# Optimization experiments

Measured on AMD Instinct MI355X. Metric: run time of the kernel, lower is better.

Reference implementation:

```python
import jax, jax.numpy as jnp
import numpy as np

NEG = -1e9  # large negative for masked logits (TRT uses dtype min)

def _rotate_every_two(x):
    # pairs (x0,x1) -> (-x1, x0), interleaved along last dim
    xr = x.reshape(*x.shape[:-1], -1, 2)
    rot = jnp.stack([-xr[..., 1], xr[..., 0]], axis=-1)
    return rot.reshape(x.shape)

def _apply_rope(x, cos, sin):
    # rot_dim == cos.shape[-1]; here it equals the full inner dim
    rot_dim = cos.shape[-1]
    x_rot, x_pass = x[..., :rot_dim], x[..., rot_dim:]
    x_rot = x_rot * cos + _rotate_every_two(x_rot) * sin
    return jnp.concatenate([x_rot, x_pass], axis=-1) if x_pass.shape[-1] else x_rot

def setup_inputs() -> dict:
    key = jax.random.key(0)
    ks = jax.random.split(key, 12)
    B, N, D_MODEL, H, DH = 2, 2048, 1024, 16, 64
    INNER = H * DH
    x = jax.random.normal(ks[0], (B, N, D_MODEL), dtype=jnp.float32)
    # rope angles: build realistic cos/sin tables repeated per head
    pos = jnp.arange(N, dtype=jnp.float32)
    inv = 1.0 / (10000.0 ** (jnp.arange(0, DH, 2, dtype=jnp.float32) / DH))
    ang = pos[:, None] * inv[None, :]              # [N, DH/2]
    ang = jnp.repeat(ang, 2, axis=-1)              # [N, DH] interleaved pairs
    ang = jnp.tile(ang, (1, H))                    # [N, INNER]
    rope_cos = jnp.broadcast_to(jnp.cos(ang)[None], (B, N, INNER)).astype(jnp.float32)
    rope_sin = jnp.broadcast_to(jnp.sin(ang)[None], (B, N, INNER)).astype(jnp.float32)
    input_lengths = jax.random.randint(ks[1], (B,), N // 2, N + 1, dtype=jnp.int32)
    s = 1.0 / np.sqrt(D_MODEL)
    Wq = jax.random.normal(ks[2], (D_MODEL, INNER), dtype=jnp.float32) * s
    bq = jnp.zeros((INNER,), jnp.float32)
    Wk = jax.random.normal(ks[3], (D_MODEL, INNER), dtype=jnp.float32) * s
    bk = jnp.zeros((INNER,), jnp.float32)
    Wv = jax.random.normal(ks[4], (D_MODEL, INNER), dtype=jnp.float32) * s
    bv = jnp.zeros((INNER,), jnp.float32)
    Wo = jax.random.normal(ks[5], (INNER, D_MODEL), dtype=jnp.float32) * (1.0 / np.sqrt(INNER))
    bo = jnp.zeros((D_MODEL,), jnp.float32)
    return {"x": x, "rope_cos": rope_cos, "rope_sin": rope_sin,
            "input_lengths": input_lengths,
            "Wq": Wq, "bq": bq, "Wk": Wk, "bk": bk, "Wv": Wv, "bv": bv,
            "Wo": Wo, "bo": bo}

def reference(x, rope_cos, rope_sin, input_lengths, Wq, bq, Wk, bk, Wv, bv, Wo, bo):
    B, N, _ = x.shape
    H, DH = 16, 64
    q = x @ Wq + bq
    k = x @ Wk + bk
    v = x @ Wv + bv
    q = _apply_rope(q, rope_cos, rope_sin)
    k = _apply_rope(k, rope_cos, rope_sin)
    # split heads: [B,N,H,DH] -> [B,H,N,DH]
    q = q.reshape(B, N, H, DH).transpose(0, 2, 1, 3)
    k = k.reshape(B, N, H, DH).transpose(0, 2, 1, 3)
    v = v.reshape(B, N, H, DH).transpose(0, 2, 1, 3)
    # NOTE: faithful to the non-plugin source path, q is NOT pre-scaled
    scores = jnp.einsum('bhqd,bhkd->bhqk', q, k)
    key_mask = jnp.arange(N)[None, :] < input_lengths[:, None]  # [B,N]
    scores = scores + jnp.where(key_mask, 0.0, NEG).astype(scores.dtype)[:, None, None, :]
    probs = jax.nn.softmax(scores, axis=-1)
    ctx = jnp.einsum('bhqk,bhkd->bhqd', probs, v)  # [B,H,N,DH]
    ctx = ctx.transpose(0, 2, 1, 3).reshape(B, N, H * DH)
    out = ctx @ Wo + bo
    out = out * key_mask[..., None].astype(out.dtype)
    return out
```

## Files before the change

kernel.cpp:

```cpp
#include <hip/hip_runtime.h>
#include <hip/hip_bf16.h>


typedef _Float16 f16x8 __attribute__((ext_vector_type(8)));
typedef float f32x4 __attribute__((ext_vector_type(4)));

#define NEGBIG (-1.0e9f)

__device__ inline f32x4 mfma16(f16x8 a, f16x8 b, f32x4 c) {
  return __builtin_amdgcn_mfma_f32_16x16x32_f16(a, b, c, 0, 0, 0);
}

__device__ inline void gload16(const void* g, void* l) {
  __builtin_amdgcn_global_load_lds(
      (const __attribute__((address_space(1))) void*)g,
      (__attribute__((address_space(3))) void*)l, 16, 0, 0);
}

__global__ __launch_bounds__(256) void prep_kernel(
    const float* __restrict__ x, const float* __restrict__ Wq,
    const float* __restrict__ Wk, const float* __restrict__ Wv,
    const float* __restrict__ Wo, _Float16* __restrict__ xh,
    _Float16* __restrict__ wt) {
  __shared__ float tile[32][33];
  const int z = blockIdx.z;
  const int tx = threadIdx.x, ty = threadIdx.y;
  if (z == 4) {
    const int bid = blockIdx.y * 32 + blockIdx.x;
    const int t = ty * 32 + tx;
#pragma unroll
    for (int i = 0; i < 4; ++i) {
      const int o = bid * 1024 + i * 256 + t;
      const float4 v = ((const float4*)x)[o];
      union { _Float16 h[4]; short4 s; } u;
      u.h[0] = (_Float16)v.x; u.h[1] = (_Float16)v.y;
      u.h[2] = (_Float16)v.z; u.h[3] = (_Float16)v.w;
      ((short4*)xh)[o] = u.s;
    }
    return;
  }
  const float* W = (z == 0) ? Wq : (z == 1) ? Wk : (z == 2) ? Wv : Wo;
  _Float16* dh = wt + (size_t)z * 1024 * 1024;
  const int j0 = blockIdx.x * 32, k0 = blockIdx.y * 32;
  for (int i = ty; i < 32; i += 8)
    tile[i][tx] = W[(size_t)(k0 + i) * 1024 + j0 + tx];
  __syncthreads();
  for (int i = ty; i < 32; i += 8)
    dh[(size_t)(j0 + i) * 1024 + k0 + tx] = (_Float16)tile[tx][i];
}


template <int TM, int EPI>
__global__ __launch_bounds__(256) void gemm_kernel(
    const _Float16* __restrict__ A, const _Float16* __restrict__ B,
    const float* __restrict__ bias0, const float* __restrict__ bias1,
    const float* __restrict__ bias2,
    const float* __restrict__ ropeC, const float* __restrict__ ropeS,
    const int* __restrict__ lens,
    _Float16* __restrict__ outQK, _Float16* __restrict__ outVT,
    float* __restrict__ outF) {
  constexpr int MI = TM / 32;
  __shared__ __align__(16) _Float16 smem[(TM + 128) * 32];
  const int t = threadIdx.x;
  const int w = t >> 6, lane = t & 63;
  const int wr = w >> 1, wc = w & 1;
  const int fr = lane & 15, fg = lane >> 4;
  const int mtile = blockIdx.x, ntile = blockIdx.y;

  const int srow = t >> 2;
  const int skel = (t & 3) << 3;
  const size_t aBase = (size_t)(mtile * TM + srow) * 1024 + skel;
  const size_t bBase = (size_t)(ntile * 128 + srow) * 1024 + skel;
  const int ldst = t * 8;
  _Float16* lA = &smem[0];
  _Float16* lB = &smem[TM * 32];

  f32x4 acc[MI][4];
#pragma unroll
  for (int i = 0; i < MI; ++i)
#pragma unroll
    for (int j = 0; j < 4; ++j) {
      acc[i][j][0] = 0.f; acc[i][j][1] = 0.f; acc[i][j][2] = 0.f; acc[i][j][3] = 0.f;
    }

  for (int k0 = 0; k0 < 1024; k0 += 32) {
    gload16(A + aBase + k0, lA + ldst);
    if constexpr (TM == 128) gload16(A + aBase + k0 + 64 * 1024, lA + ldst + 2048);
    gload16(B + bBase + k0, lB + ldst);
    gload16(B + bBase + k0 + 64 * 1024, lB + ldst + 2048);
    __syncthreads();

    f16x8 af[MI], bf[4];
#pragma unroll
    for (int mi = 0; mi < MI; ++mi)
      af[mi] = *(const f16x8*)&lA[(wr * (TM / 2) + mi * 16 + fr) * 32 + fg * 8];
#pragma unroll
    for (int ni = 0; ni < 4; ++ni)
      bf[ni] = *(const f16x8*)&lB[(wc * 64 + ni * 16 + fr) * 32 + fg * 8];
#pragma unroll
    for (int mi = 0; mi < MI; ++mi)
#pragma unroll
      for (int ni = 0; ni < 4; ++ni)
        acc[mi][ni] = mfma16(af[mi], bf[ni], acc[mi][ni]);
    __syncthreads();
  }

  const int rowbase = mtile * TM + wr * (TM / 2);
  const int colbase = ntile * 128 + wc * 64;

  if constexpr (EPI == 0) {
    const int which = colbase >> 10;
    if (which < 2) {
      const float* bias = which ? bias1 : bias0;
#pragma unroll
      for (int ni = 0; ni < 4; ++ni) {
        const int gcol = colbase + ni * 16 + fr;
        const int jj = gcol & 1023;
        const int hh = jj >> 6, dd = jj & 63;
        const float bv = bias[jj];
#pragma unroll
        for (int mi = 0; mi < MI; ++mi) {
#pragma unroll
          for (int r = 0; r < 4; ++r) {
            const int grow = rowbase + mi * 16 + fg * 4 + r;
            const int b = grow >> 11, n = grow & 2047;
            float val = acc[mi][ni][r] + bv;
            float part = __shfl_xor(val, 1);
            const size_t ro = (size_t)(b * 2048 + n) * 1024 + jj;
            const float c = ropeC[ro], s = ropeS[ro];
            float rot = (fr & 1) ? (val * c + part * s) : (val * c - part * s);
            if (!which) rot *= 1.44269504f;
            outQK[((size_t)((which * 2 + b) * 16 + hh) * 2048 + n) * 64 + dd] =
                (_Float16)rot;
          }
        }
      }
    } else {
#pragma unroll
      for (int ni = 0; ni < 4; ++ni) {
        const int gcol = colbase + ni * 16 + fr;
        const int jj = gcol & 1023;
        const int hh = jj >> 6, dd = jj & 63;
        const float bv = bias2[jj];
#pragma unroll
        for (int mi = 0; mi < MI; ++mi) {
          const int n0 = rowbase + mi * 16 + fg * 4;
          const int b = n0 >> 11, n = n0 & 2047;
          union { _Float16 h[4]; short4 s4; } u;
#pragma unroll
          for (int r = 0; r < 4; ++r) u.h[r] = (_Float16)(acc[mi][ni][r] + bv);
          *(short4*)(outVT + ((size_t)(b * 16 + hh) * 64 + dd) * 2048 + n) = u.s4;
        }
      }
    }
  } else {
    const int b = rowbase >> 11;
    const int len = lens[b];
#pragma unroll
    for (int ni = 0; ni < 4; ++ni) {
      const int gcol = colbase + ni * 16 + fr;
      const float bv = bias0[gcol];
#pragma unroll
      for (int mi = 0; mi < MI; ++mi) {
#pragma unroll
        for (int r = 0; r < 4; ++r) {
          const int m = rowbase + mi * 16 + fg * 4 + r;
          const int n = m & 2047;
          float val = acc[mi][ni][r] + bv;
          if (n >= len) val = 0.f;
          outF[(size_t)m * 1024 + gcol] = val;
        }
      }
    }
  }
}

__global__ __launch_bounds__(128, 4) void attn_kernel(
    const _Float16* __restrict__ qk, const _Float16* __restrict__ vt,
    const int* __restrict__ lens, _Float16* __restrict__ ctx) {
  __shared__ __align__(16) char lds[18432];
  const int t = threadIdx.x;
  const int w = t >> 6, lane = t & 63;
  const int fr = lane & 15, fg = lane >> 4;
  const int qtile = blockIdx.x, bh = blockIdx.y;
  const int b = bh >> 4, h = bh & 15;
  const int len = lens[b];
  const int q0 = qtile * 32 + w * 16;
  const size_t qoff = (size_t)(b * 16 + h) * 2048 * 64;
  const size_t koff = (size_t)((2 + b) * 16 + h) * 2048 * 64;
  const size_t voff = (size_t)(b * 16 + h) * 64 * 2048;

  f16x8 qf[2];
#pragma unroll
  for (int s = 0; s < 2; ++s)
    qf[s] = *(const f16x8*)(qk + qoff + (size_t)(q0 + fr) * 64 + s * 32 + fg * 8);

  f16x8 onef;
#pragma unroll
  for (int i = 0; i < 8; ++i) onef[i] = (_Float16)1.0f;

  const int skey = t >> 3;
  const int soct = (t & 7) ^ (skey & 7);
  const size_t kg = koff + (size_t)skey * 64 + soct * 8;
  const int sd = t >> 2;
  const int svo = (t & 3) ^ ((sd >> 1) & 3);
  const size_t vg = voff + (size_t)sd * 2048 + svo * 8;
  char* pb = lds + 16384 + w * 1024;

  f32x4 o_acc[4];
#pragma unroll
  for (int dt = 0; dt < 4; ++dt) {
    o_acc[dt][0] = 0.f; o_acc[dt][1] = 0.f; o_acc[dt][2] = 0.f; o_acc[dt][3] = 0.f;
  }
  f32x4 lacc;
  lacc[0] = 0.f; lacc[1] = 0.f; lacc[2] = 0.f; lacc[3] = 0.f;
  float mrun = -1e30f;

#define STAGE(bi, k0_) do { \
    char* dst = lds + (bi) * 8192 + t * 16; \
    gload16(qk + kg + (size_t)(k0_) * 64, dst); \
    gload16(qk + kg + (size_t)(k0_) * 64 + 1024, dst + 2048); \
    gload16(vt + vg + (k0_), dst + 4096); \
    gload16(vt + vg + (k0_) + 32 * 2048, dst + 6144); \
  } while (0)

  const int nkb = (len + 31) >> 5;
  STAGE(0, 0);

  for (int kb = 0; kb < nkb; ++kb) {
    const int cur = kb & 1;
    if (kb + 1 < nkb) {
      STAGE(cur ^ 1, (kb + 1) * 32);
      asm volatile("s_waitcnt vmcnt(4)" ::: "memory");
    } else {
      asm volatile("s_waitcnt vmcnt(0)" ::: "memory");
    }
    __builtin_amdgcn_s_barrier();

    const char* Kb = lds + cur * 8192;
    const char* Vb = Kb + 4096;

    f32x4 sacc[2];
#pragma unroll
    for (int ct = 0; ct < 2; ++ct) {
      sacc[ct][0] = 0.f; sacc[ct][1] = 0.f; sacc[ct][2] = 0.f; sacc[ct][3] = 0.f;
    }
    __builtin_amdgcn_s_setprio(1);
#pragma unroll
    for (int ct = 0; ct < 2; ++ct) {
      const int krow = ct * 16 + fr;
      const int swz = (krow & 7) << 4;
#pragma unroll
      for (int s = 0; s < 2; ++s) {
        const f16x8 kf = *(const f16x8*)(Kb + ((krow * 128 + s * 64 + fg * 16) ^ swz));
        sacc[ct] = mfma16(kf, qf[s], sacc[ct]);
      }
    }
    __builtin_amdgcn_s_setprio(0);

    if ((kb == nkb - 1) && (len & 31)) {
#pragma unroll
      for (int ct = 0; ct < 2; ++ct)
#pragma unroll
        for (int r = 0; r < 4; ++r)
          if (kb * 32 + ct * 16 + fg * 4 + r >= len) sacc[ct][r] = NEGBIG;
    }

    float mx = fmaxf(fmaxf(fmaxf(sacc[0][0], sacc[0][1]), fmaxf(sacc[0][2], sacc[0][3])),
                     fmaxf(fmaxf(sacc[1][0], sacc[1][1]), fmaxf(sacc[1][2], sacc[1][3])));
    mx = fmaxf(mx, __shfl_xor(mx, 16));
    mx = fmaxf(mx, __shfl_xor(mx, 32));
    if (!__all(mx <= mrun + 8.f)) {
      const float mnew = fmaxf(mrun, mx);
      const float scq = exp2f(mrun - mnew);
      mrun = mnew;
      float scrow[4];
#pragma unroll
      for (int r = 0; r < 4; ++r) scrow[r] = __shfl(scq, fg * 4 + r);
      lacc[0] *= scrow[0]; lacc[1] *= scrow[1];
      lacc[2] *= scrow[2]; lacc[3] *= scrow[3];
#pragma unroll
      for (int dt = 0; dt < 4; ++dt) {
        o_acc[dt][0] *= scrow[0]; o_acc[dt][1] *= scrow[1];
        o_acc[dt][2] *= scrow[2]; o_acc[dt][3] *= scrow[3];
      }
    }
    float p[2][4];
#pragma unroll
    for (int ct = 0; ct < 2; ++ct)
#pragma unroll
      for (int r = 0; r < 4; ++r) p[ct][r] = exp2f(sacc[ct][r] - mrun);

    const int pswz = ((fr >> 1) & 3) << 4;
#pragma unroll
    for (int ct = 0; ct < 2; ++ct) {
      union { _Float16 h[4]; uint2 u2; } pk;
      pk.h[0] = (_Float16)p[ct][0]; pk.h[1] = (_Float16)p[ct][1];
      pk.h[2] = (_Float16)p[ct][2]; pk.h[3] = (_Float16)p[ct][3];
      *(uint2*)(pb + ((fr * 64 + ct * 32 + fg * 8) ^ pswz)) = pk.u2;
    }
    const f16x8 pf = *(const f16x8*)(pb + ((fr * 64 + fg * 16) ^ pswz));

    __builtin_amdgcn_s_setprio(1);
#pragma unroll
    for (int dt = 0; dt < 4; ++dt) {
      const int d = dt * 16 + fr;
      const f16x8 vf =
          *(const f16x8*)(Vb + ((d * 64 + (fg ^ ((d >> 1) & 3)) * 16)));
      o_acc[dt] = mfma16(pf, vf, o_acc[dt]);
    }
    lacc = mfma16(pf, onef, lacc);
    __builtin_amdgcn_s_setprio(0);

    asm volatile("" ::: "memory");
    __builtin_amdgcn_s_barrier();
  }
#undef STAGE

  float linv[4];
#pragma unroll
  for (int r = 0; r < 4; ++r) linv[r] = 1.f / lacc[r];
#pragma unroll
  for (int dt = 0; dt < 4; ++dt)
#pragma unroll
    for (int r = 0; r < 4; ++r) {
      const int n = q0 + fg * 4 + r;
      ctx[(size_t)(b * 2048 + n) * 1024 + h * 64 + dt * 16 + fr] =
          (_Float16)(o_acc[dt][r] * linv[r]);
    }
}


extern "C" void kernel_launch(void* const* d_in, const int* in_sizes, int n_in,
                              void* d_out, int out_size, void* d_ws, size_t ws_size,
                              hipStream_t stream) {
  const float* x = (const float*)d_in[0];
  const float* rc = (const float*)d_in[1];
  const float* rs = (const float*)d_in[2];
  const int* lens = (const int*)d_in[3];
  const float* Wq = (const float*)d_in[4];
  const float* bq = (const float*)d_in[5];
  const float* Wk = (const float*)d_in[6];
  const float* bk = (const float*)d_in[7];
  const float* Wv = (const float*)d_in[8];
  const float* bv = (const float*)d_in[9];
  const float* Wo = (const float*)d_in[10];
  const float* bo = (const float*)d_in[11];
  float* out = (float*)d_out;

  char* ws = (char*)d_ws;
  const size_t MB = 1024 * 1024;
  _Float16* XH = (_Float16*)(ws + 0);
  _Float16* WT = (_Float16*)(ws + 8 * MB);
  _Float16* QK = (_Float16*)(ws + 16 * MB);
  _Float16* VT = (_Float16*)(ws + 32 * MB);
  _Float16* CTX = (_Float16*)(ws + 40 * MB);

  prep_kernel<<<dim3(32, 32, 5), dim3(32, 8), 0, stream>>>(x, Wq, Wk, Wv, Wo,
                                                           XH, WT);
  gemm_kernel<128, 0><<<dim3(32, 24), 256, 0, stream>>>(
      XH, WT, bq, bk, bv, rc, rs, nullptr, QK, VT, nullptr);
  attn_kernel<<<dim3(64, 32), 128, 0, stream>>>(QK, VT, lens, CTX);
  gemm_kernel<64, 2><<<dim3(64, 8), 256, 0, stream>>>(
      CTX, WT + (size_t)3 * 1024 * 1024, bo, nullptr, nullptr, nullptr,
      nullptr, lens, nullptr, nullptr, out);
}
```

Baseline: 165.0 us.

## Rewrite attention with 32x32 MFMA tiles, register-resident P and larger key blocks

The attention kernel moves from 16x16x32 to 32x32x16 MFMA, with each wave handling 32 queries and 64-key blocks. The P matrix is built in registers with packed fp16 conversion and lane-exchange shuffles instead of going through LDS. The row sum is accumulated with scalar adds instead of an MFMA against a ones vector. The grid is flattened and remapped so that 8 heads share a query-tile ordering. This is meant to cut LDS traffic and MFMA issue overhead, but it raises register and LDS use, lowers occupancy bounds (launch_bounds 4→2), and halves the block count.

```diff
diff --git a/kernel.cpp b/kernel.cpp
--- a/kernel.cpp
+++ b/kernel.cpp
@@ -2,19 +2,30 @@
 #include <hip/hip_bf16.h>
 
 
+typedef __fp16 fp16x2 __attribute__((ext_vector_type(2)));
 typedef _Float16 f16x8 __attribute__((ext_vector_type(8)));
 typedef float f32x4 __attribute__((ext_vector_type(4)));
+typedef float f32x16 __attribute__((ext_vector_type(16)));
 
 #define NEGBIG (-1.0e9f)
 
 __device__ inline f32x4 mfma16(f16x8 a, f16x8 b, f32x4 c) {
   return __builtin_amdgcn_mfma_f32_16x16x32_f16(a, b, c, 0, 0, 0);
+}
+__device__ inline f32x16 mfma32(f16x8 a, f16x8 b, f32x16 c) {
+  return __builtin_amdgcn_mfma_f32_32x32x16_f16(a, b, c, 0, 0, 0);
 }
 
 __device__ inline void gload16(const void* g, void* l) {
   __builtin_amdgcn_global_load_lds(
       (const __attribute__((address_space(1))) void*)g,
       (__attribute__((address_space(3))) void*)l, 16, 0, 0);
+}
+
+__device__ inline unsigned pk2u(float a, float b) {
+  union { fp16x2 h; unsigned u; } x;
+  x.h = __builtin_amdgcn_cvt_pkrtz(a, b);
+  return x.u;
 }
 
 __global__ __launch_bounds__(256) void prep_kernel(
@@ -48,7 +59,6 @@
   for (int i = ty; i < 32; i += 8)
     dh[(size_t)(j0 + i) * 1024 + k0 + tx] = (_Float16)tile[tx][i];
 }
-
 
 template <int TM, int EPI>
 __global__ __launch_bounds__(256) void gemm_kernel(
@@ -175,141 +185,153 @@
   }
 }
 
-__global__ __launch_bounds__(128, 4) void attn_kernel(
+__global__ __launch_bounds__(128, 2) void attn_kernel(
     const _Float16* __restrict__ qk, const _Float16* __restrict__ vt,
     const int* __restrict__ lens, _Float16* __restrict__ ctx) {
-  __shared__ __align__(16) char lds[18432];
+  __shared__ __align__(16) char lds[32768];
   const int t = threadIdx.x;
   const int w = t >> 6, lane = t & 63;
-  const int fr = lane & 15, fg = lane >> 4;
-  const int qtile = blockIdx.x, bh = blockIdx.y;
+  const int lq = lane & 31, hi = lane >> 5;
+  const int fid = blockIdx.x;
+  const int qtile = (fid >> 3) & 31;
+  const int bh = (fid & 7) + ((fid >> 8) << 3);
   const int b = bh >> 4, h = bh & 15;
   const int len = lens[b];
-  const int q0 = qtile * 32 + w * 16;
+  const int q0w = qtile * 64 + w * 32;
   const size_t qoff = (size_t)(b * 16 + h) * 2048 * 64;
   const size_t koff = (size_t)((2 + b) * 16 + h) * 2048 * 64;
   const size_t voff = (size_t)(b * 16 + h) * 64 * 2048;
 
-  f16x8 qf[2];
-#pragma unroll
-  for (int s = 0; s < 2; ++s)
-    qf[s] = *(const f16x8*)(qk + qoff + (size_t)(q0 + fr) * 64 + s * 32 + fg * 8);
-
-  f16x8 onef;
-#pragma unroll
-  for (int i = 0; i < 8; ++i) onef[i] = (_Float16)1.0f;
-
-  const int skey = t >> 3;
-  const int soct = (t & 7) ^ (skey & 7);
-  const size_t kg = koff + (size_t)skey * 64 + soct * 8;
-  const int sd = t >> 2;
-  const int svo = (t & 3) ^ ((sd >> 1) & 3);
-  const size_t vg = voff + (size_t)sd * 2048 + svo * 8;
-  char* pb = lds + 16384 + w * 1024;
-
-  f32x4 o_acc[4];
-#pragma unroll
-  for (int dt = 0; dt < 4; ++dt) {
-    o_acc[dt][0] = 0.f; o_acc[dt][1] = 0.f; o_acc[dt][2] = 0.f; o_acc[dt][3] = 0.f;
-  }
-  f32x4 lacc;
-  lacc[0] = 0.f; lacc[1] = 0.f; lacc[2] = 0.f; lacc[3] = 0.f;
-  float mrun = -1e30f;
+  f16x8 qf[4];
+#pragma unroll
+  for (int ks = 0; ks < 4; ++ks)
+    qf[ks] = *(const f16x8*)(qk + qoff + (size_t)(q0w + lq) * 64 + ks * 16 + hi * 8);
+
+  const int srow = t >> 3;
+  const int sslot = (t & 7) ^ (srow & 7);
+  const size_t kg = koff + (size_t)srow * 64 + sslot * 8;
+  const size_t vg = voff + (size_t)srow * 2048 + sslot * 8;
+
+  f32x16 o0, o1;
+#pragma unroll
+  for (int i = 0; i < 16; ++i) { o0[i] = 0.f; o1[i] = 0.f; }
+  float mrun = -1e30f, lsum = 0.f;
 
 #define STAGE(bi, k0_) do { \
-    char* dst = lds + (bi) * 8192 + t * 16; \
-    gload16(qk + kg + (size_t)(k0_) * 64, dst); \
-    gload16(qk + kg + (size_t)(k0_) * 64 + 1024, dst + 2048); \
-    gload16(vt + vg + (k0_), dst + 4096); \
-    gload16(vt + vg + (k0_) + 32 * 2048, dst + 6144); \
+    char* dst = lds + (bi) * 16384 + t * 16; \
+    const _Float16* ks_ = qk + kg + (size_t)(k0_) * 64; \
+    const _Float16* vs_ = vt + vg + (k0_); \
+    gload16(ks_, dst); gload16(ks_ + 1024, dst + 2048); \
+    gload16(ks_ + 2048, dst + 4096); gload16(ks_ + 3072, dst + 6144); \
+    gload16(vs_, dst + 8192); gload16(vs_ + 32768, dst + 10240); \
+    gload16(vs_ + 65536, dst + 12288); gload16(vs_ + 98304, dst + 14336); \
   } while (0)
 
-  const int nkb = (len + 31) >> 5;
+  const int nkb = (len + 63) >> 6;
   STAGE(0, 0);
 
   for (int kb = 0; kb < nkb; ++kb) {
     const int cur = kb & 1;
     if (kb + 1 < nkb) {
-      STAGE(cur ^ 1, (kb + 1) * 32);
-      asm volatile("s_waitcnt vmcnt(4)" ::: "memory");
+      STAGE(cur ^ 1, (kb + 1) * 64);
+      asm volatile("s_waitcnt vmcnt(8)" ::: "memory");
     } else {
       asm volatile("s_waitcnt vmcnt(0)" ::: "memory");
     }
     __builtin_amdgcn_s_barrier();
 
-    const char* Kb = lds + cur * 8192;
-    const char* Vb = Kb + 4096;
-
-    f32x4 sacc[2];
-#pragma unroll
-    for (int ct = 0; ct < 2; ++ct) {
-      sacc[ct][0] = 0.f; sacc[ct][1] = 0.f; sacc[ct][2] = 0.f; sacc[ct][3] = 0.f;
-    }
+    const char* Kb = lds + cur * 16384;
+    const char* Vb = Kb + 8192;
+    const int rsw = (lq & 7) << 4;
+
+    f32x16 s0, s1;
+#pragma unroll
+    for (int i = 0; i < 16; ++i) { s0[i] = 0.f; s1[i] = 0.f; }
     __builtin_amdgcn_s_setprio(1);
 #pragma unroll
-    for (int ct = 0; ct < 2; ++ct) {
-      const int krow = ct * 16 + fr;
-      const int swz = (krow & 7) << 4;
-#pragma unroll
-      for (int s = 0; s < 2; ++s) {
-        const f16x8 kf = *(const f16x8*)(Kb + ((krow * 128 + s * 64 + fg * 16) ^ swz));
-        sacc[ct] = mfma16(kf, qf[s], sacc[ct]);
+    for (int ks = 0; ks < 4; ++ks) {
+      const int col = ks * 32 + hi * 16;
+      const f16x8 k0f = *(const f16x8*)(Kb + lq * 128 + (col ^ rsw));
+      const f16x8 k1f = *(const f16x8*)(Kb + (32 + lq) * 128 + (col ^ rsw));
+      s0 = mfma32(k0f, qf[ks], s0);
+      s1 = mfma32(k1f, qf[ks], s1);
+    }
+    __builtin_amdgcn_s_setprio(0);
+
+    if (kb == nkb - 1 && (len & 63)) {
+#pragma unroll
+      for (int r = 0; r < 16; ++r) {
+        const int key = kb * 64 + (r & 3) + ((r >> 2) << 3) + hi * 4;
+        if (key >= len) s0[r] = NEGBIG;
+        if (key + 32 >= len) s1[r] = NEGBIG;
       }
     }
-    __builtin_amdgcn_s_setprio(0);
-
-    if ((kb == nkb - 1) && (len & 31)) {
-#pragma unroll
-      for (int ct = 0; ct < 2; ++ct)
-#pragma unroll
-        for (int r = 0; r < 4; ++r)
-          if (kb * 32 + ct * 16 + fg * 4 + r >= len) sacc[ct][r] = NEGBIG;
-    }
-
-    float mx = fmaxf(fmaxf(fmaxf(sacc[0][0], sacc[0][1]), fmaxf(sacc[0][2], sacc[0][3])),
-                     fmaxf(fmaxf(sacc[1][0], sacc[1][1]), fmaxf(sacc[1][2], sacc[1][3])));
-    mx = fmaxf(mx, __shfl_xor(mx, 16));
+
+    float mx = s0[0];
+#pragma unroll
+    for (int r = 1; r < 16; ++r) mx = fmaxf(mx, s0[r]);
+#pragma unroll
+    for (int r = 0; r < 16; ++r) mx = fmaxf(mx, s1[r]);
     mx = fmaxf(mx, __shfl_xor(mx, 32));
+
     if (!__all(mx <= mrun + 8.f)) {
       const float mnew = fmaxf(mrun, mx);
       const float scq = exp2f(mrun - mnew);
       mrun = mnew;
-      float scrow[4];
-#pragma unroll
-      for (int r = 0; r < 4; ++r) scrow[r] = __shfl(scq, fg * 4 + r);
-      lacc[0] *= scrow[0]; lacc[1] *= scrow[1];
-      lacc[2] *= scrow[2]; lacc[3] *= scrow[3];
-#pragma unroll
-      for (int dt = 0; dt < 4; ++dt) {
-        o_acc[dt][0] *= scrow[0]; o_acc[dt][1] *= scrow[1];
-        o_acc[dt][2] *= scrow[2]; o_acc[dt][3] *= scrow[3];
-      }
-    }
-    float p[2][4];
-#pragma unroll
-    for (int ct = 0; ct < 2; ++ct)
-#pragma unroll
-      for (int r = 0; r < 4; ++r) p[ct][r] = exp2f(sacc[ct][r] - mrun);
-
-    const int pswz = ((fr >> 1) & 3) << 4;
-#pragma unroll
-    for (int ct = 0; ct < 2; ++ct) {
-      union { _Float16 h[4]; uint2 u2; } pk;
-      pk.h[0] = (_Float16)p[ct][0]; pk.h[1] = (_Float16)p[ct][1];
-      pk.h[2] = (_Float16)p[ct][2]; pk.h[3] = (_Float16)p[ct][3];
-      *(uint2*)(pb + ((fr * 64 + ct * 32 + fg * 8) ^ pswz)) = pk.u2;
-    }
-    const f16x8 pf = *(const f16x8*)(pb + ((fr * 64 + fg * 16) ^ pswz));
+      lsum *= scq;
+      float sc[16];
+#pragma unroll
+      for (int r = 0; r < 16; ++r)
+        sc[r] = __shfl(scq, (r & 3) + ((r >> 2) << 3) + hi * 4);
+#pragma unroll
+      for (int r = 0; r < 16; ++r) { o0[r] *= sc[r]; o1[r] *= sc[r]; }
+    }
+
+    unsigned W[16];
+    float ps = 0.f;
+#pragma unroll
+    for (int u = 0; u < 4; ++u) {
+      const float p0 = exp2f(s0[4 * u + 0] - mrun);
+      const float p1 = exp2f(s0[4 * u + 1] - mrun);
+      const float p2 = exp2f(s0[4 * u + 2] - mrun);
+      const float p3 = exp2f(s0[4 * u + 3] - mrun);
+      ps += (p0 + p1) + (p2 + p3);
+      W[2 * u] = pk2u(p0, p1);
+      W[2 * u + 1] = pk2u(p2, p3);
+    }
+#pragma unroll
+    for (int u = 0; u < 4; ++u) {
+      const float p0 = exp2f(s1[4 * u + 0] - mrun);
+      const float p1 = exp2f(s1[4 * u + 1] - mrun);
+      const float p2 = exp2f(s1[4 * u + 2] - mrun);
+      const float p3 = exp2f(s1[4 * u + 3] - mrun);
+      ps += (p0 + p1) + (p2 + p3);
+      W[8 + 2 * u] = pk2u(p0, p1);
+      W[8 + 2 * u + 1] = pk2u(p2, p3);
+    }
+    ps += __shfl_xor(ps, 32);
+    lsum += ps;
 
     __builtin_amdgcn_s_setprio(1);
 #pragma unroll
-    for (int dt = 0; dt < 4; ++dt) {
-      const int d = dt * 16 + fr;
-      const f16x8 vf =
-          *(const f16x8*)(Vb + ((d * 64 + (fg ^ ((d >> 1) & 3)) * 16)));
-      o_acc[dt] = mfma16(pf, vf, o_acc[dt]);
-    }
-    lacc = mfma16(pf, onef, lacc);
+    for (int ks = 0; ks < 4; ++ks) {
+      const unsigned w0 = W[4 * ks + 0], w1 = W[4 * ks + 1];
+      const unsigned w2 = W[4 * ks + 2], w3 = W[4 * ks + 3];
+      const unsigned sendA = hi ? w0 : w2;
+      const unsigned sendB = hi ? w1 : w3;
+      const unsigned recvA = __shfl_xor(sendA, 32);
+      const unsigned recvB = __shfl_xor(sendB, 32);
+      union { unsigned u[4]; f16x8 v; } af;
+      af.u[0] = hi ? recvA : w0;
+      af.u[1] = hi ? recvB : w1;
+      af.u[2] = hi ? w2 : recvA;
+      af.u[3] = hi ? w3 : recvB;
+      const int col = ks * 32 + hi * 16;
+      const f16x8 v0f = *(const f16x8*)(Vb + lq * 128 + (col ^ rsw));
+      const f16x8 v1f = *(const f16x8*)(Vb + (32 + lq) * 128 + (col ^ rsw));
+      o0 = mfma32(af.v, v0f, o0);
+      o1 = mfma32(af.v, v1f, o1);
+    }
     __builtin_amdgcn_s_setprio(0);
 
     asm volatile("" ::: "memory");
@@ -317,17 +339,16 @@
   }
 #undef STAGE
 
-  float linv[4];
-#pragma unroll
-  for (int r = 0; r < 4; ++r) linv[r] = 1.f / lacc[r];
-#pragma unroll
-  for (int dt = 0; dt < 4; ++dt)
-#pragma unroll
-    for (int r = 0; r < 4; ++r) {
-      const int n = q0 + fg * 4 + r;
-      ctx[(size_t)(b * 2048 + n) * 1024 + h * 64 + dt * 16 + fr] =
-          (_Float16)(o_acc[dt][r] * linv[r]);
-    }
+  const float li = 1.f / lsum;
+#pragma unroll
+  for (int r = 0; r < 16; ++r) {
+    const int qr = (r & 3) + ((r >> 2) << 3) + hi * 4;
+    const float lr = __shfl(li, qr);
+    const int n = q0w + qr;
+    _Float16* dst = ctx + (size_t)(b * 2048 + n) * 1024 + h * 64;
+    dst[lq] = (_Float16)(o0[r] * lr);
+    dst[32 + lq] = (_Float16)(o1[r] * lr);
+  }
 }
 
 
@@ -360,7 +381,7 @@
                                                            XH, WT);
   gemm_kernel<128, 0><<<dim3(32, 24), 256, 0, stream>>>(
       XH, WT, bq, bk, bv, rc, rs, nullptr, QK, VT, nullptr);
-  attn_kernel<<<dim3(64, 32), 128, 0, stream>>>(QK, VT, lens, CTX);
+  attn_kernel<<<1024, 128, 0, stream>>>(QK, VT, lens, CTX);
   gemm_kernel<64, 2><<<dim3(64, 8), 256, 0, stream>>>(
       CTX, WT + (size_t)3 * 1024 * 1024, bo, nullptr, nullptr, nullptr,
       nullptr, lens, nullptr, nullptr, out);
```

Measured after the change: 169.6 us. 1.03x slower.
